# Kernel tuning notes

Hardware: AMD Instinct MI355X
Metric: run time of the kernel (lower is better)

Reference implementation:

```python
import jax, jax.numpy as jnp
import numpy as np

H = 16  # hidden size (fixed by the module)


def setup_inputs() -> dict:
    key = jax.random.key(0)
    ks = jax.random.split(key, 12)
    B, T = 512, 4096
    x = jax.random.normal(ks[0], (B, T, 1), dtype=jnp.float32)
    h0 = jax.random.normal(ks[1], (B, H), dtype=jnp.float32)
    c0 = jax.random.normal(ks[2], (B, H), dtype=jnp.float32)
    s = 1.0 / np.sqrt(H)
    # PyTorch LSTM params, gate order (i, f, g, o)
    W_ih = jax.random.uniform(ks[3], (4 * H, 1), jnp.float32, -s, s)
    W_hh = jax.random.uniform(ks[4], (4 * H, H), jnp.float32, -s, s)
    b_ih = jax.random.uniform(ks[5], (4 * H,), jnp.float32, -s, s)
    b_hh = jax.random.uniform(ks[6], (4 * H,), jnp.float32, -s, s)
    # MLP head: Linear(16,16) then Linear(16,1)
    W1 = jax.random.uniform(ks[7], (H, H), jnp.float32, -s, s)
    b1 = jax.random.uniform(ks[8], (H,), jnp.float32, -s, s)
    W2 = jax.random.uniform(ks[9], (1, H), jnp.float32, -s, s)
    b2 = jax.random.uniform(ks[10], (1,), jnp.float32, -s, s)
    return {"x": x, "h0": h0, "c0": c0, "W_ih": W_ih, "W_hh": W_hh,
            "b_ih": b_ih, "b_hh": b_hh, "W1": W1, "b1": b1,
            "W2": W2, "b2": b2, "batch_size": B}


def _lstm(x, h0, c0, W_ih, W_hh, b):
    # x: [B,T,1] -> scan over time; gate order i,f,g,o (PyTorch)
    xs = jnp.swapaxes(x, 0, 1)  # [T,B,1]
    # precompute input projection for all timesteps: [T,B,4H]
    xg = jnp.einsum('tbi,gi->tbg', xs, W_ih) + b

    def step(carry, xg_t):
        h, c = carry
        gates = xg_t + h @ W_hh.T  # [B,4H]
        i, f, g, o = jnp.split(gates, 4, axis=-1)
        c = jax.nn.sigmoid(f) * c + jax.nn.sigmoid(i) * jnp.tanh(g)
        h = jax.nn.sigmoid(o) * jnp.tanh(c)
        return (h, c), h

    _, hs = jax.lax.scan(step, (h0, c0), xg)
    return jnp.swapaxes(hs, 0, 1)  # [B,T,H]


def reference(x, h0, c0, W_ih, W_hh, b_ih, b_hh, W1, b1, W2, b2, batch_size):
    hs = _lstm(x, h0, c0, W_ih, W_hh, b_ih + b_hh)  # [B,T,H]
    y = jax.nn.relu(hs)
    y = jax.nn.relu(y @ W1.T + b1)
    y = jnp.tanh(y @ W2.T + b2)  # [B,T,1]
    T = x.shape[1]
    out = y.reshape(batch_size, 1, T)
    return jnp.cumsum(out, axis=1)  # cumsum over singleton dim (faithful to source)
```

## Files before the change

kernel.cpp:

```cpp
#include <hip/hip_runtime.h>
#include <cstdint>
#include <cstddef>

#define LOG2E 1.4426950408889634f

__device__ __forceinline__ float fexp2(float x) {
#if __has_builtin(__builtin_amdgcn_exp2f)
  return __builtin_amdgcn_exp2f(x);
#else
  return exp2f(x);
#endif
}

__device__ __forceinline__ float frcp(float x) {
#if __has_builtin(__builtin_amdgcn_rcpf)
  return __builtin_amdgcn_rcpf(x);
#else
  return 1.0f / x;
#endif
}

__device__ __forceinline__ float rl(float v, int l) {
  return __int_as_float(__builtin_amdgcn_readlane(__float_as_int(v), l));
}

__global__ __launch_bounds__(64) void lstm_gen_kernel(
    const float* __restrict__ x, const float* __restrict__ h0,
    const float* __restrict__ c0, const float* __restrict__ W_ih,
    const float* __restrict__ W_hh, const float* __restrict__ b_ih,
    const float* __restrict__ b_hh, const float* __restrict__ W1,
    const float* __restrict__ b1, const float* __restrict__ W2,
    const float* __restrict__ b2, float* __restrict__ out, int T) {
  const int b = blockIdx.x;
  const int lane = threadIdx.x;
  const int j = lane & 15;
  const int type = lane >> 4;

  __shared__ float hbuf[4 * 80];

  const float sk = (type == 2) ? (-2.0f * LOG2E) : (-LOG2E);
  const float Aact = (type == 2) ? 2.0f : 1.0f;
  const float Bact = (type == 2) ? -1.0f : 0.0f;

  float w[16];
#pragma unroll
  for (int jj = 0; jj < 16; ++jj) w[jj] = W_hh[lane * 16 + jj] * sk;
  const float wi = W_ih[lane] * sk;
  const float bk = (b_ih[lane] + b_hh[lane]) * sk;

  float w1r[16];
#pragma unroll
  for (int jj = 0; jj < 16; ++jj) w1r[jj] = W1[j * 16 + jj];
  const float b1r = b1[j];
  const float w2r = W2[j];
  const float b2v = b2[0];

  float h = h0[b * 16 + j];
  float c = c0[b * 16 + j];

  const float* xrow = x + (size_t)b * (size_t)T;
  float* orow = out + (size_t)b * (size_t)T;
  const int T4 = T >> 2;
  const float4* xrow4 = (const float4*)xrow;

  float4 xa = xrow4[0];
  float4 xb = xrow4[(1 < T4) ? 1 : 0];
  float4 xc2 = xrow4[(2 < T4) ? 2 : 0];

#pragma unroll 1
  for (int t4i = 0; t4i < T4; ++t4i) {
    const float4 xcur = xa;
    xa = xb;
    xb = xc2;
    int nidx = t4i + 3;
    nidx = (nidx < T4) ? nidx : (T4 - 1);
    xc2 = xrow4[nidx];

#pragma unroll
    for (int tt = 0; tt < 4; ++tt) {
      const float xv = (tt == 0) ? xcur.x : (tt == 1) ? xcur.y
                        : (tt == 2) ? xcur.z : xcur.w;
      float a0 = fmaf(wi, xv, bk);
      float a1 = 0.0f, a2 = 0.0f, a3 = 0.0f;
#pragma unroll
      for (int jj = 0; jj < 16; jj += 4) {
        a0 = fmaf(rl(h, jj + 0), w[jj + 0], a0);
        a1 = fmaf(rl(h, jj + 1), w[jj + 1], a1);
        a2 = fmaf(rl(h, jj + 2), w[jj + 2], a2);
        a3 = fmaf(rl(h, jj + 3), w[jj + 3], a3);
      }
      const float gacc = (a0 + a1) + (a2 + a3);
      const float act = fmaf(Aact, frcp(1.0f + fexp2(gacc)), Bact);

      const float iv = __shfl(act, j);
      const float fv = __shfl(act, j + 16);
      const float gv = __shfl(act, j + 32);
      const float ov = __shfl(act, j + 48);

      c = fmaf(fv, c, iv * gv);
      const float tc = fmaf(-2.0f, frcp(1.0f + fexp2(c * (2.0f * LOG2E))), 1.0f);
      h = ov * tc;
      hbuf[tt * 80 + lane] = h;
    }

    const int q = type;
    const float4 hA = *(const float4*)&hbuf[q * 80 + 0];
    const float4 hB = *(const float4*)&hbuf[q * 80 + 4];
    const float4 hC = *(const float4*)&hbuf[q * 80 + 8];
    const float4 hD = *(const float4*)&hbuf[q * 80 + 12];

    float m0 = fmaf(fmaxf(hA.x, 0.0f), w1r[0], b1r);
    float m1 = fmaxf(hA.y, 0.0f) * w1r[1];
    float m2 = fmaxf(hA.z, 0.0f) * w1r[2];
    float m3 = fmaxf(hA.w, 0.0f) * w1r[3];
    m0 = fmaf(fmaxf(hB.x, 0.0f), w1r[4], m0);
    m1 = fmaf(fmaxf(hB.y, 0.0f), w1r[5], m1);
    m2 = fmaf(fmaxf(hB.z, 0.0f), w1r[6], m2);
    m3 = fmaf(fmaxf(hB.w, 0.0f), w1r[7], m3);
    m0 = fmaf(fmaxf(hC.x, 0.0f), w1r[8], m0);
    m1 = fmaf(fmaxf(hC.y, 0.0f), w1r[9], m1);
    m2 = fmaf(fmaxf(hC.z, 0.0f), w1r[10], m2);
    m3 = fmaf(fmaxf(hC.w, 0.0f), w1r[11], m3);
    m0 = fmaf(fmaxf(hD.x, 0.0f), w1r[12], m0);
    m1 = fmaf(fmaxf(hD.y, 0.0f), w1r[13], m1);
    m2 = fmaf(fmaxf(hD.z, 0.0f), w1r[14], m2);
    m3 = fmaf(fmaxf(hD.w, 0.0f), w1r[15], m3);
    const float y2 = (m0 + m1) + (m2 + m3);
    const float y2r = fmaxf(y2, 0.0f);

    float v = y2r * w2r;
    v += __shfl_xor(v, 1);
    v += __shfl_xor(v, 2);
    v += __shfl_xor(v, 4);
    v += __shfl_xor(v, 8);
    const float z = v + b2v;
    const float y3 = 1.0f - 2.0f * frcp(1.0f + fexp2(z * (2.0f * LOG2E)));

    if (j == 0) orow[t4i * 4 + q] = y3;
  }
}

extern "C" void kernel_launch(void* const* d_in, const int* in_sizes, int n_in,
                              void* d_out, int out_size, void* d_ws,
                              size_t ws_size, hipStream_t stream) {
  (void)n_in; (void)d_ws; (void)ws_size;
  const float* x = (const float*)d_in[0];
  const float* h0 = (const float*)d_in[1];
  const float* c0 = (const float*)d_in[2];
  const float* W_ih = (const float*)d_in[3];
  const float* W_hh = (const float*)d_in[4];
  const float* b_ih = (const float*)d_in[5];
  const float* b_hh = (const float*)d_in[6];
  const float* W1 = (const float*)d_in[7];
  const float* b1 = (const float*)d_in[8];
  const float* W2 = (const float*)d_in[9];
  const float* b2 = (const float*)d_in[10];

  const int B = in_sizes[1] / 16;
  const int T = in_sizes[0] / (B > 0 ? B : 1);

  lstm_gen_kernel<<<B, 64, 0, stream>>>(x, h0, c0, W_ih, W_hh, b_ih, b_hh,
                                        W1, b1, W2, b2, (float*)d_out, T);
}
```

Before: 1.044 ms.

## Replace LDS shuffles and shared buffer with permlane swaps and DPP moves

The per-step gate gather, which used four __shfl calls (ds_bpermute through LDS), is replaced by permlane16/permlane32 swap reductions. These combine i*g, f and o across 16-lane rows directly in registers. The MLP head no longer stages h through a shared-memory buffer. Each row keeps its own timestep's h and computes the 16x16 matvec with DPP row rotations against pre-rotated W1 weights, and the final 16-lane sum uses DPP quad/mirror moves. The aim is to cut LDS latency from the serial recurrence path, at the cost of relying on gfx950-specific permlane swap instructions and more complex lane bookkeeping.

New measurement: 1.167 ms. +11.8%, slower.

```diff
diff --git a/kernel.cpp b/kernel.cpp
--- a/kernel.cpp
+++ b/kernel.cpp
@@ -22,6 +22,54 @@
 
 __device__ __forceinline__ float rl(float v, int l) {
   return __int_as_float(__builtin_amdgcn_readlane(__float_as_int(v), l));
+}
+
+template <int CTRL>
+__device__ __forceinline__ float dppmov(float x) {
+  return __int_as_float(
+      __builtin_amdgcn_update_dpp(0, __float_as_int(x), CTRL, 0xf, 0xf, true));
+}
+#define DPP_QUAD_XOR1 0xB1
+#define DPP_QUAD_XOR2 0x4E
+#define DPP_HALF_MIRR 0x141
+#define DPP_MIRR 0x140
+#define DPP_ROR1 0x121
+#define DPP_ROR4 0x124
+#define DPP_ROR8 0x128
+#define DPP_ROR12 0x12C
+
+__device__ __forceinline__ float sum16(float x) {
+#if __has_builtin(__builtin_amdgcn_permlane16_swap)
+  auto r = __builtin_amdgcn_permlane16_swap(__float_as_uint(x),
+                                            __float_as_uint(x), false, false);
+  return __uint_as_float(r[0]) + __uint_as_float(r[1]);
+#else
+  float a = x, b = x;
+  asm("v_permlane16_swap_b32 %0, %1" : "+v"(a), "+v"(b));
+  return a + b;
+#endif
+}
+__device__ __forceinline__ float sum32(float x) {
+#if __has_builtin(__builtin_amdgcn_permlane32_swap)
+  auto r = __builtin_amdgcn_permlane32_swap(__float_as_uint(x),
+                                            __float_as_uint(x), false, false);
+  return __uint_as_float(r[0]) + __uint_as_float(r[1]);
+#else
+  float a = x, b = x;
+  asm("v_permlane32_swap_b32 %0, %1" : "+v"(a), "+v"(b));
+  return a + b;
+#endif
+}
+__device__ __forceinline__ float mul32(float x) {
+#if __has_builtin(__builtin_amdgcn_permlane32_swap)
+  auto r = __builtin_amdgcn_permlane32_swap(__float_as_uint(x),
+                                            __float_as_uint(x), false, false);
+  return __uint_as_float(r[0]) * __uint_as_float(r[1]);
+#else
+  float a = x, b = x;
+  asm("v_permlane32_swap_b32 %0, %1" : "+v"(a), "+v"(b));
+  return a * b;
+#endif
 }
 
 __global__ __launch_bounds__(64) void lstm_gen_kernel(
@@ -35,8 +83,9 @@
   const int lane = threadIdx.x;
   const int j = lane & 15;
   const int type = lane >> 4;
-
-  __shared__ float hbuf[4 * 80];
+  const bool rowodd = (lane & 16) != 0;
+  const bool isF = (type == 1);
+  const bool isO = (type == 3);
 
   const float sk = (type == 2) ? (-2.0f * LOG2E) : (-LOG2E);
   const float Aact = (type == 2) ? 2.0f : 1.0f;
@@ -48,9 +97,9 @@
   const float wi = W_ih[lane] * sk;
   const float bk = (b_ih[lane] + b_hh[lane]) * sk;
 
-  float w1r[16];
-#pragma unroll
-  for (int jj = 0; jj < 16; ++jj) w1r[jj] = W1[j * 16 + jj];
+  float w1rot[16];
+#pragma unroll
+  for (int r = 0; r < 16; ++r) w1rot[r] = W1[j * 16 + ((j - r) & 15)];
   const float b1r = b1[j];
   const float w2r = W2[j];
   const float b2v = b2[0];
@@ -76,6 +125,8 @@
     nidx = (nidx < T4) ? nidx : (T4 - 1);
     xc2 = xrow4[nidx];
 
+    float hq = 0.0f;
+
 #pragma unroll
     for (int tt = 0; tt < 4; ++tt) {
       const float xv = (tt == 0) ? xcur.x : (tt == 1) ? xcur.y
@@ -92,51 +143,48 @@
       const float gacc = (a0 + a1) + (a2 + a3);
       const float act = fmaf(Aact, frcp(1.0f + fexp2(gacc)), Bact);
 
-      const float iv = __shfl(act, j);
-      const float fv = __shfl(act, j + 16);
-      const float gv = __shfl(act, j + 32);
-      const float ov = __shfl(act, j + 48);
-
-      c = fmaf(fv, c, iv * gv);
+      const float m = mul32(act);
+      const float IG_all = sum16(rowodd ? 0.0f : m);
+      const float F_all = sum32(sum16(isF ? act : 0.0f));
+      const float O_all = sum32(sum16(isO ? act : 0.0f));
+
+      c = fmaf(F_all, c, IG_all);
       const float tc = fmaf(-2.0f, frcp(1.0f + fexp2(c * (2.0f * LOG2E))), 1.0f);
-      h = ov * tc;
-      hbuf[tt * 80 + lane] = h;
+      h = O_all * tc;
+      hq = (type == tt) ? h : hq;
     }
 
-    const int q = type;
-    const float4 hA = *(const float4*)&hbuf[q * 80 + 0];
-    const float4 hB = *(const float4*)&hbuf[q * 80 + 4];
-    const float4 hC = *(const float4*)&hbuf[q * 80 + 8];
-    const float4 hD = *(const float4*)&hbuf[q * 80 + 12];
-
-    float m0 = fmaf(fmaxf(hA.x, 0.0f), w1r[0], b1r);
-    float m1 = fmaxf(hA.y, 0.0f) * w1r[1];
-    float m2 = fmaxf(hA.z, 0.0f) * w1r[2];
-    float m3 = fmaxf(hA.w, 0.0f) * w1r[3];
-    m0 = fmaf(fmaxf(hB.x, 0.0f), w1r[4], m0);
-    m1 = fmaf(fmaxf(hB.y, 0.0f), w1r[5], m1);
-    m2 = fmaf(fmaxf(hB.z, 0.0f), w1r[6], m2);
-    m3 = fmaf(fmaxf(hB.w, 0.0f), w1r[7], m3);
-    m0 = fmaf(fmaxf(hC.x, 0.0f), w1r[8], m0);
-    m1 = fmaf(fmaxf(hC.y, 0.0f), w1r[9], m1);
-    m2 = fmaf(fmaxf(hC.z, 0.0f), w1r[10], m2);
-    m3 = fmaf(fmaxf(hC.w, 0.0f), w1r[11], m3);
-    m0 = fmaf(fmaxf(hD.x, 0.0f), w1r[12], m0);
-    m1 = fmaf(fmaxf(hD.y, 0.0f), w1r[13], m1);
-    m2 = fmaf(fmaxf(hD.z, 0.0f), w1r[14], m2);
-    m3 = fmaf(fmaxf(hD.w, 0.0f), w1r[15], m3);
+    const float cur = fmaxf(hq, 0.0f);
+    float r0v = cur;
+    float r4v = dppmov<DPP_ROR4>(cur);
+    float r8v = dppmov<DPP_ROR8>(cur);
+    float r12v = dppmov<DPP_ROR12>(cur);
+    float m0 = fmaf(r0v, w1rot[0], b1r);
+    float m1 = r4v * w1rot[4];
+    float m2 = r8v * w1rot[8];
+    float m3 = r12v * w1rot[12];
+#pragma unroll
+    for (int r = 1; r < 4; ++r) {
+      r0v = dppmov<DPP_ROR1>(r0v);
+      r4v = dppmov<DPP_ROR1>(r4v);
+      r8v = dppmov<DPP_ROR1>(r8v);
+      r12v = dppmov<DPP_ROR1>(r12v);
+      m0 = fmaf(r0v, w1rot[r], m0);
+      m1 = fmaf(r4v, w1rot[4 + r], m1);
+      m2 = fmaf(r8v, w1rot[8 + r], m2);
+      m3 = fmaf(r12v, w1rot[12 + r], m3);
+    }
     const float y2 = (m0 + m1) + (m2 + m3);
-    const float y2r = fmaxf(y2, 0.0f);
-
-    float v = y2r * w2r;
-    v += __shfl_xor(v, 1);
-    v += __shfl_xor(v, 2);
-    v += __shfl_xor(v, 4);
-    v += __shfl_xor(v, 8);
+
+    float v = fmaxf(y2, 0.0f) * w2r;
+    v += dppmov<DPP_QUAD_XOR1>(v);
+    v += dppmov<DPP_QUAD_XOR2>(v);
+    v += dppmov<DPP_HALF_MIRR>(v);
+    v += dppmov<DPP_MIRR>(v);
     const float z = v + b2v;
-    const float y3 = 1.0f - 2.0f * frcp(1.0f + fexp2(z * (2.0f * LOG2E)));
-
-    if (j == 0) orow[t4i * 4 + q] = y3;
+    const float y3 = fmaf(-2.0f, frcp(1.0f + fexp2(z * (2.0f * LOG2E))), 1.0f);
+
+    if (j == 0) orow[t4i * 4 + type] = y3;
   }
 }
 
```
